# Optimization experiments

Hardware: AMD Instinct MI355X
Metric: run time of the kernel (lower is better)

The kernel has to match this reference:

```python
import math
import jax, jax.numpy as jnp
import numpy as np

SEQ, BATCH, HID, N_HEAD = 1024, 8, 1024, 16


def setup_inputs() -> dict:
    key0 = jax.random.key(0)
    ks = jax.random.split(key0, 7)
    shp = (SEQ, BATCH, HID)
    w = lambda k: jax.random.normal(k, (HID, HID), dtype=jnp.float32) * 0.02
    return {
        "value": jax.random.normal(ks[0], shp, dtype=jnp.float32),
        "key": jax.random.normal(ks[1], shp, dtype=jnp.float32),
        "query": jax.random.normal(ks[2], shp, dtype=jnp.float32),
        "Wq": w(ks[3]), "Wk": w(ks[4]), "Wv": w(ks[5]), "Wo": w(ks[6]),
    }


def _proj_split(x, W, n_head, d_k):
    # x: (S,B,H) -> linear -> split heads -> stack heads along batch dim: (S, n_head*B, d_k)
    S, B, H = x.shape
    p = x @ W.T                                   # (S,B,H)
    p = p.reshape(S, B, n_head, d_k)
    p = p.transpose(0, 2, 1, 3).reshape(S, n_head * B, d_k)
    return p


def reference(value, key, query, Wq, Wk, Wv, Wo):
    S, B, H = value.shape
    n_head = N_HEAD
    d_k = H // n_head
    Q = _proj_split(query, Wq, n_head, d_k)       # (S, n_head*B, d_k)
    K = _proj_split(key, Wk, n_head, d_k)
    V = _proj_split(value, Wv, n_head, d_k)
    # scores[b,i,j] = K_i . Q_j / sqrt(d_k)  (note: rows = key index, cols = query index)
    scores = jnp.einsum('ibd,jbd->bij', K, Q) / math.sqrt(d_k)  # (n_head*B, S, S)
    future_mask = jnp.triu(jnp.ones((S, S), dtype=bool), 1)      # True where j > i
    scores = jnp.where(future_mask[None, :, :], -jnp.inf, scores)
    # faithful to original: softmax over dim=2 (the QUERY axis)
    dist = jax.nn.softmax(scores, axis=2)                         # (n_head*B, S, S)
    # att[j,b,d] = sum_i dist[b,i,j] * V[i,b,d]
    att = jnp.einsum('bij,ibd->jbd', dist, V)                     # (S, n_head*B, d_k)
    # un-stack heads: (S, n_head, B, d_k) -> (B, S, n_head*d_k)
    att = att.reshape(S, n_head, B, d_k).transpose(2, 0, 1, 3).reshape(B, S, H)
    out = (att @ Wo.T).transpose(1, 0, 2)                         # (S, B, H)
    return out, dist
```

## Files before the change

### kernel.cpp

```cpp
#include <hip/hip_runtime.h>
#include <hip/hip_bf16.h>
#include <stdint.h>

#define SQ   1024
#define NB   8
#define HD   1024
#define NHD  16
#define DKK  64

typedef __bf16 bf16x8_t __attribute__((ext_vector_type(8)));
typedef float  f32x4_t  __attribute__((ext_vector_type(4)));
typedef __hip_bfloat16 bf16;

__device__ __forceinline__ void gld_lds16(const void* g, void* l) {
    __builtin_amdgcn_global_load_lds(
        (__attribute__((address_space(1))) void*)const_cast<void*>(g),
        (__attribute__((address_space(3))) void*)l,
        16, 0, 0);
}

__device__ __forceinline__ bf16x8_t cvt8(float4 a, float4 b) {
    bf16x8_t r;
    r[0] = (__bf16)a.x; r[1] = (__bf16)a.y; r[2] = (__bf16)a.z; r[3] = (__bf16)a.w;
    r[4] = (__bf16)b.x; r[5] = (__bf16)b.y; r[6] = (__bf16)b.z; r[7] = (__bf16)b.w;
    return r;
}

__global__ __launch_bounds__(256, 2)
void gemm_kernel(const void* __restrict__ A0, const void* __restrict__ A1,
                 const void* __restrict__ A2,
                 const float* __restrict__ W0, const float* __restrict__ W1,
                 const float* __restrict__ W2,
                 void* __restrict__ O0, void* __restrict__ O1,
                 void* __restrict__ O2, int mode)
{
    const int z = blockIdx.z;
    const void*  A  = (z == 0) ? A0 : (z == 1) ? A1 : A2;
    const float* Wf = (z == 0) ? W0 : (z == 1) ? W1 : W2;
    void*        Ov = (z == 0) ? O0 : (z == 1) ? O1 : O2;

    __shared__ alignas(16) bf16 lA[128 * 32];
    __shared__ alignas(16) bf16 lB[128 * 32];

    const int tid  = threadIdx.x;
    const int lane = tid & 63;
    const int w    = tid >> 6;
    const int wr   = w >> 1;
    const int wc   = w & 1;
    const int g    = lane >> 4;
    const int ln   = lane & 15;
    const int bm   = blockIdx.y;
    const int bn   = blockIdx.x;

    f32x4_t acc[4][4];
#pragma unroll
    for (int i = 0; i < 4; ++i)
#pragma unroll
        for (int j = 0; j < 4; ++j)
            acc[i][j] = (f32x4_t){0.f, 0.f, 0.f, 0.f};

    const size_t arow0 = (size_t)bm * 128;
    const size_t brow0 = (size_t)bn * 128;
    const float* Af  = (const float*)A;
    const bf16*  Ab  = (const bf16*)A;

    for (int k0 = 0; k0 < HD; k0 += 32) {
#pragma unroll
        for (int q = 0; q < 2; ++q) {
            const int cid = (q * 4 + w) * 64 + lane;
            const int r   = cid >> 2;
            const int gch = (cid & 3) ^ ((r ^ (r >> 2)) & 3);
            if (mode == 0) {
                const float4* src = (const float4*)(Af + (arow0 + r) * HD + k0 + gch * 8);
                *(bf16x8_t*)&lA[cid * 8] = cvt8(src[0], src[1]);
            } else {
                gld_lds16((const char*)Ab + ((arow0 + r) * HD + k0) * 2 + gch * 16,
                          (char*)lA + cid * 16);
            }
            const float4* wsrc = (const float4*)(Wf + (brow0 + r) * HD + k0 + gch * 8);
            *(bf16x8_t*)&lB[cid * 8] = cvt8(wsrc[0], wsrc[1]);
        }
        __syncthreads();
        bf16x8_t av[4], bv[4];
#pragma unroll
        for (int mi = 0; mi < 4; ++mi) {
            const int row = wr * 64 + mi * 16 + ln;
            av[mi] = *(const bf16x8_t*)&lA[row * 32 + ((g ^ ((row ^ (row >> 2)) & 3)) << 3)];
        }
#pragma unroll
        for (int ni = 0; ni < 4; ++ni) {
            const int row = wc * 64 + ni * 16 + ln;
            bv[ni] = *(const bf16x8_t*)&lB[row * 32 + ((g ^ ((row ^ (row >> 2)) & 3)) << 3)];
        }
#pragma unroll
        for (int mi = 0; mi < 4; ++mi)
#pragma unroll
            for (int ni = 0; ni < 4; ++ni)
                acc[mi][ni] = __builtin_amdgcn_mfma_f32_16x16x32_bf16(
                    av[mi], bv[ni], acc[mi][ni], 0, 0, 0);
        __syncthreads();
    }

    bf16*  Ob = (bf16*)Ov;
    float* Of = (float*)Ov;
#pragma unroll
    for (int mi = 0; mi < 4; ++mi) {
#pragma unroll
        for (int ni = 0; ni < 4; ++ni) {
            const int o = bn * 128 + wc * 64 + ni * 16 + ln;
#pragma unroll
            for (int r = 0; r < 4; ++r) {
                const int m = bm * 128 + wr * 64 + mi * 16 + g * 4 + r;
                const float v = acc[mi][ni][r];
                if (mode == 0) {
                    const int h = o >> 6, d = o & 63;
                    const int s = m >> 3, b = m & 7;
                    Ob[(((size_t)(h * 8 + b) * SQ + s) << 6) + d] = __float2bfloat16(v);
                } else {
                    Of[(size_t)m * HD + o] = v;
                }
            }
        }
    }
}

__global__ __launch_bounds__(256, 2)
void scores_softmax_kernel(const bf16* __restrict__ Kh, const bf16* __restrict__ Qh,
                           float* __restrict__ Dist)
{
    __shared__ alignas(16) bf16 Kl[64 * 64];
    __shared__ alignas(16) bf16 Ql[64 * 64];
    const int tid = threadIdx.x, lane = tid & 63, w = tid >> 6;
    const int g = lane >> 4, ln = lane & 15;
    const int ib = blockIdx.x, bh = blockIdx.y;
    const char* Kp = (const char*)(Kh + ((size_t)bh * SQ + ib * 64) * DKK);
    const char* Qp = (const char*)(Qh + (size_t)bh * SQ * DKK);
    float* Dp = Dist + (size_t)bh * SQ * SQ;

#pragma unroll
    for (int q = 0; q < 2; ++q) {
        const int cid = (q * 4 + w) * 64 + lane;
        const int r   = cid >> 3;
        const int cc  = (cid & 7) ^ ((r ^ (r >> 3)) & 7);
        gld_lds16(Kp + r * 128 + cc * 16, (char*)Kl + cid * 16);
    }
    __syncthreads();
    const int arow = w * 16 + ln;
    const int asw  = (arow ^ (arow >> 3)) & 7;
    const bf16x8_t ak0 = *(const bf16x8_t*)&Kl[arow * 64 + ((g ^ asw) << 3)];
    const bf16x8_t ak1 = *(const bf16x8_t*)&Kl[arow * 64 + (((4 + g) ^ asw) << 3)];

    const int irow = ib * 64 + w * 16 + g * 4;

    auto stage_q = [&](int jt) {
#pragma unroll
        for (int q = 0; q < 2; ++q) {
            const int cid = (q * 4 + w) * 64 + lane;
            const int r   = cid >> 3;
            const int cc  = (cid & 7) ^ ((r ^ (r >> 3)) & 7);
            gld_lds16(Qp + (size_t)jt * 8192 + r * 128 + cc * 16, (char*)Ql + cid * 16);
        }
    };
    auto compute_tile = [&](f32x4_t* accp) {
#pragma unroll
        for (int nf = 0; nf < 4; ++nf) {
            const int brow = nf * 16 + ln;
            const int bsw  = (brow ^ (brow >> 3)) & 7;
            bf16x8_t b0 = *(const bf16x8_t*)&Ql[brow * 64 + ((g ^ bsw) << 3)];
            bf16x8_t b1 = *(const bf16x8_t*)&Ql[brow * 64 + (((4 + g) ^ bsw) << 3)];
            f32x4_t a = (f32x4_t){0.f, 0.f, 0.f, 0.f};
            a = __builtin_amdgcn_mfma_f32_16x16x32_bf16(ak0, b0, a, 0, 0, 0);
            a = __builtin_amdgcn_mfma_f32_16x16x32_bf16(ak1, b1, a, 0, 0, 0);
            accp[nf] = a;
        }
    };

    float lsum[4] = {0.f, 0.f, 0.f, 0.f};
    for (int jt = 0; jt <= ib; ++jt) {
        __syncthreads();
        stage_q(jt);
        __syncthreads();
        f32x4_t acc[4];
        compute_tile(acc);
        float part[4] = {0.f, 0.f, 0.f, 0.f};
#pragma unroll
        for (int nf = 0; nf < 4; ++nf) {
            const int j = jt * 64 + nf * 16 + ln;
#pragma unroll
            for (int r = 0; r < 4; ++r) {
                const float s = acc[nf][r] * 0.125f;
                part[r] += (j <= irow + r) ? __expf(s) : 0.f;
            }
        }
#pragma unroll
        for (int r = 0; r < 4; ++r) {
            float p = part[r];
            p += __shfl_xor(p, 1);
            p += __shfl_xor(p, 2);
            p += __shfl_xor(p, 4);
            p += __shfl_xor(p, 8);
            lsum[r] += p;
        }
    }
    float inv[4];
#pragma unroll
    for (int r = 0; r < 4; ++r) inv[r] = 1.f / lsum[r];

    for (int jt = 0; jt < 16; ++jt) {
        if (jt <= ib) {
            __syncthreads();
            stage_q(jt);
            __syncthreads();
            f32x4_t acc[4];
            compute_tile(acc);
#pragma unroll
            for (int nf = 0; nf < 4; ++nf) {
                const int j = jt * 64 + nf * 16 + ln;
#pragma unroll
                for (int r = 0; r < 4; ++r) {
                    const float e = (j <= irow + r)
                        ? __expf(acc[nf][r] * 0.125f) * inv[r] : 0.f;
                    Dp[(size_t)(irow + r) * SQ + j] = e;
                }
            }
        } else {
            const uint4 zz = make_uint4(0u, 0u, 0u, 0u);
#pragma unroll
            for (int q = 0; q < 4; ++q) {
                const int cid = q * 256 + tid;
                const int row = cid >> 4;
                float* p = Dp + (size_t)(ib * 64 + row) * SQ + jt * 64 + (cid & 15) * 4;
                *(uint4*)p = zz;
            }
        }
    }
}

__global__ __launch_bounds__(256, 2)
void att_v_kernel(const float* __restrict__ Dist, const bf16* __restrict__ Vh,
                  bf16* __restrict__ att4)
{
    __shared__ alignas(16) bf16 dT[64 * 72];
    __shared__ alignas(16) bf16 vT[64 * 72];
    const int tid = threadIdx.x, lane = tid & 63, w = tid >> 6;
    const int g = lane >> 4, ln = lane & 15;
    const int jb = blockIdx.x, bh = blockIdx.y;
    const float* Dp = Dist + (size_t)bh * SQ * SQ;
    const bf16*  Vp = Vh + (size_t)bh * SQ * DKK;

    f32x4_t acc[4];
#pragma unroll
    for (int nf = 0; nf < 4; ++nf) acc[nf] = (f32x4_t){0.f, 0.f, 0.f, 0.f};

    unsigned short* dTs = (unsigned short*)dT;
    unsigned short* vTs = (unsigned short*)vT;

    for (int it = jb; it < 16; ++it) {
        __syncthreads();
#pragma unroll
        for (int q = 0; q < 4; ++q) {
            const int cid = q * 256 + tid;
            const int i   = cid >> 4;
            const int jc  = (cid & 15) * 4;
            float4 dv = *(const float4*)(Dp + ((size_t)(it * 64 + i) * SQ + jb * 64 + jc));
            const float de[4] = {dv.x, dv.y, dv.z, dv.w};
#pragma unroll
            for (int e = 0; e < 4; ++e) {
                const int j   = jc + e;
                const int isw = i ^ (((j >> 3) & 7) << 3);
                bf16 bv = __float2bfloat16(de[e]);
                dTs[j * 72 + isw] = *(unsigned short*)&bv;
            }
        }
#pragma unroll
        for (int q = 0; q < 2; ++q) {
            const int cid = q * 256 + tid;
            const int i   = cid >> 3;
            const int dc  = (cid & 7) * 8;
            uint4 vvec = *(const uint4*)(Vp + ((size_t)(it * 64 + i) * DKK + dc));
            const unsigned short* vs = (const unsigned short*)&vvec;
#pragma unroll
            for (int e = 0; e < 8; ++e) {
                const int d   = dc + e;
                const int isw = i ^ (((d >> 3) & 7) << 3);
                vTs[d * 72 + isw] = vs[e];
            }
        }
        __syncthreads();
#pragma unroll
        for (int kk = 0; kk < 2; ++kk) {
            const int arow  = w * 16 + ln;
            const int abase = (kk * 32 + g * 8) ^ (((arow >> 3) & 7) << 3);
            bf16x8_t a = *(const bf16x8_t*)&dT[arow * 72 + abase];
#pragma unroll
            for (int nf = 0; nf < 4; ++nf) {
                const int brow  = nf * 16 + ln;
                const int bbase = (kk * 32 + g * 8) ^ (((brow >> 3) & 7) << 3);
                bf16x8_t b = *(const bf16x8_t*)&vT[brow * 72 + bbase];
                acc[nf] = __builtin_amdgcn_mfma_f32_16x16x32_bf16(a, b, acc[nf], 0, 0, 0);
            }
        }
    }
    const int h = bh >> 3, b = bh & 7;
#pragma unroll
    for (int nf = 0; nf < 4; ++nf) {
#pragma unroll
        for (int r = 0; r < 4; ++r) {
            const int j = jb * 64 + w * 16 + g * 4 + r;
            att4[(size_t)(j * 8 + b) * HD + h * 64 + nf * 16 + ln] =
                __float2bfloat16(acc[nf][r]);
        }
    }
}

extern "C" void kernel_launch(void* const* d_in, const int* in_sizes, int n_in,
                              void* d_out, int out_size, void* d_ws, size_t ws_size,
                              hipStream_t stream)
{
    const float* value = (const float*)d_in[0];
    const float* key_  = (const float*)d_in[1];
    const float* query = (const float*)d_in[2];
    const float* Wq    = (const float*)d_in[3];
    const float* Wk    = (const float*)d_in[4];
    const float* Wv    = (const float*)d_in[5];
    const float* Wo    = (const float*)d_in[6];

    float* out  = (float*)d_out;
    float* dist = out + (size_t)SQ * NB * HD;

    char* ws   = (char*)d_ws;
    bf16* Qh   = (bf16*)(ws);
    bf16* Kh   = (bf16*)(ws + (size_t)16 * 1024 * 1024);
    bf16* Vh   = (bf16*)(ws + (size_t)32 * 1024 * 1024);
    bf16* att4 = (bf16*)(ws + (size_t)48 * 1024 * 1024);

    dim3 blk(256);
    gemm_kernel<<<dim3(8, 64, 3), blk, 0, stream>>>(
        query, key_, value, Wq, Wk, Wv, Qh, Kh, Vh, 0);
    scores_softmax_kernel<<<dim3(16, 128), blk, 0, stream>>>(Kh, Qh, dist);
    att_v_kernel<<<dim3(16, 128), blk, 0, stream>>>(dist, Vh, att4);
    gemm_kernel<<<dim3(8, 64, 1), blk, 0, stream>>>(
        att4, att4, att4, Wo, Wo, Wo, out, out, out, 1);
}
```

Measured before the change: 1.007 ms.

## Fuse dist computation with PV, double-buffer GEMM and attention staging

The separate scores+softmax write and att_v read of the fp32 dist matrix are replaced by a rowsum kernel that computes only inverse row sums, plus a fused kernel that recomputes scores per column block, writes dist, and immediately multiplies by V through LDS. V is stored transposed by the projection GEMM, so the PV kernel can stage it without a per-element transpose. The GEMM gains register-prefetched double buffering, and the attention kernels double-buffer Q/K/V tiles. The cost is recomputing the QK scores and more LDS per block. The inverse row sums are parked in the output buffer, which the final GEMM later overwrites.

```diff
diff --git a/kernel.cpp b/kernel.cpp
--- a/kernel.cpp
+++ b/kernel.cpp
@@ -9,6 +9,7 @@
 #define DKK  64
 
 typedef __bf16 bf16x8_t __attribute__((ext_vector_type(8)));
+typedef __bf16 bf16x4_t __attribute__((ext_vector_type(4)));
 typedef float  f32x4_t  __attribute__((ext_vector_type(4)));
 typedef __hip_bfloat16 bf16;
 
@@ -24,6 +25,17 @@
     r[0] = (__bf16)a.x; r[1] = (__bf16)a.y; r[2] = (__bf16)a.z; r[3] = (__bf16)a.w;
     r[4] = (__bf16)b.x; r[5] = (__bf16)b.y; r[6] = (__bf16)b.z; r[7] = (__bf16)b.w;
     return r;
+}
+
+__device__ __forceinline__ void stage64(const char* gbase, int rowstride,
+                                        char* lbase, int w, int lane) {
+#pragma unroll
+    for (int q = 0; q < 2; ++q) {
+        const int cid = (q * 4 + w) * 64 + lane;
+        const int r   = cid >> 3;
+        const int cc  = (cid & 7) ^ ((r ^ (r >> 3)) & 7);
+        gld_lds16(gbase + r * rowstride + cc * 16, lbase + cid * 16);
+    }
 }
 
 __global__ __launch_bounds__(256, 2)
@@ -39,8 +51,8 @@
     const float* Wf = (z == 0) ? W0 : (z == 1) ? W1 : W2;
     void*        Ov = (z == 0) ? O0 : (z == 1) ? O1 : O2;
 
-    __shared__ alignas(16) bf16 lA[128 * 32];
-    __shared__ alignas(16) bf16 lB[128 * 32];
+    __shared__ alignas(16) bf16 lA[2][128 * 32];
+    __shared__ alignas(16) bf16 lB[2][128 * 32];
 
     const int tid  = threadIdx.x;
     const int lane = tid & 63;
@@ -61,36 +73,69 @@
 
     const size_t arow0 = (size_t)bm * 128;
     const size_t brow0 = (size_t)bn * 128;
-    const float* Af  = (const float*)A;
-    const bf16*  Ab  = (const bf16*)A;
-
-    for (int k0 = 0; k0 < HD; k0 += 32) {
+    const float* Af = (const float*)A;
+    const bf16*  Ab = (const bf16*)A;
+
+    int scid[2], srow[2], sch[2];
+#pragma unroll
+    for (int q = 0; q < 2; ++q) {
+        const int cid = (q * 4 + w) * 64 + lane;
+        scid[q] = cid;
+        srow[q] = cid >> 2;
+        sch[q]  = (cid & 3) ^ ((srow[q] ^ (srow[q] >> 2)) & 3);
+    }
+
+    float4 pa[4], pw[4];
+
+    auto issue_loads = [&](int k0, int buf) {
 #pragma unroll
         for (int q = 0; q < 2; ++q) {
-            const int cid = (q * 4 + w) * 64 + lane;
-            const int r   = cid >> 2;
-            const int gch = (cid & 3) ^ ((r ^ (r >> 2)) & 3);
-            if (mode == 0) {
-                const float4* src = (const float4*)(Af + (arow0 + r) * HD + k0 + gch * 8);
-                *(bf16x8_t*)&lA[cid * 8] = cvt8(src[0], src[1]);
-            } else {
-                gld_lds16((const char*)Ab + ((arow0 + r) * HD + k0) * 2 + gch * 16,
-                          (char*)lA + cid * 16);
+            const float4* wsrc = (const float4*)(Wf + (brow0 + srow[q]) * HD + k0 + sch[q] * 8);
+            pw[q * 2]     = wsrc[0];
+            pw[q * 2 + 1] = wsrc[1];
+        }
+        if (mode == 0) {
+#pragma unroll
+            for (int q = 0; q < 2; ++q) {
+                const float4* asrc = (const float4*)(Af + (arow0 + srow[q]) * HD + k0 + sch[q] * 8);
+                pa[q * 2]     = asrc[0];
+                pa[q * 2 + 1] = asrc[1];
             }
-            const float4* wsrc = (const float4*)(Wf + (brow0 + r) * HD + k0 + gch * 8);
-            *(bf16x8_t*)&lB[cid * 8] = cvt8(wsrc[0], wsrc[1]);
-        }
-        __syncthreads();
+        } else {
+#pragma unroll
+            for (int q = 0; q < 2; ++q)
+                gld_lds16((const char*)Ab + ((arow0 + srow[q]) * HD + k0) * 2 + sch[q] * 16,
+                          (char*)&lA[buf][0] + scid[q] * 16);
+        }
+    };
+    auto commit_writes = [&](int buf) {
+#pragma unroll
+        for (int q = 0; q < 2; ++q)
+            *(bf16x8_t*)&lB[buf][scid[q] * 8] = cvt8(pw[q * 2], pw[q * 2 + 1]);
+        if (mode == 0) {
+#pragma unroll
+            for (int q = 0; q < 2; ++q)
+                *(bf16x8_t*)&lA[buf][scid[q] * 8] = cvt8(pa[q * 2], pa[q * 2 + 1]);
+        }
+    };
+
+    issue_loads(0, 0);
+    commit_writes(0);
+    __syncthreads();
+
+    int cur = 0;
+    for (int ks = 0; ks < 32; ++ks) {
+        if (ks < 31) issue_loads((ks + 1) * 32, cur ^ 1);
         bf16x8_t av[4], bv[4];
 #pragma unroll
         for (int mi = 0; mi < 4; ++mi) {
             const int row = wr * 64 + mi * 16 + ln;
-            av[mi] = *(const bf16x8_t*)&lA[row * 32 + ((g ^ ((row ^ (row >> 2)) & 3)) << 3)];
+            av[mi] = *(const bf16x8_t*)&lA[cur][row * 32 + ((g ^ ((row ^ (row >> 2)) & 3)) << 3)];
         }
 #pragma unroll
         for (int ni = 0; ni < 4; ++ni) {
             const int row = wc * 64 + ni * 16 + ln;
-            bv[ni] = *(const bf16x8_t*)&lB[row * 32 + ((g ^ ((row ^ (row >> 2)) & 3)) << 3)];
+            bv[ni] = *(const bf16x8_t*)&lB[cur][row * 32 + ((g ^ ((row ^ (row >> 2)) & 3)) << 3)];
         }
 #pragma unroll
         for (int mi = 0; mi < 4; ++mi)
@@ -98,7 +143,9 @@
             for (int ni = 0; ni < 4; ++ni)
                 acc[mi][ni] = __builtin_amdgcn_mfma_f32_16x16x32_bf16(
                     av[mi], bv[ni], acc[mi][ni], 0, 0, 0);
+        if (ks < 31) commit_writes(cur ^ 1);
         __syncthreads();
+        cur ^= 1;
     }
 
     bf16*  Ob = (bf16*)Ov;
@@ -115,7 +162,10 @@
                 if (mode == 0) {
                     const int h = o >> 6, d = o & 63;
                     const int s = m >> 3, b = m & 7;
-                    Ob[(((size_t)(h * 8 + b) * SQ + s) << 6) + d] = __float2bfloat16(v);
+                    if (z == 2)
+                        Ob[((size_t)((h * 8 + b) * DKK + d)) * SQ + s] = __float2bfloat16(v);
+                    else
+                        Ob[(((size_t)(h * 8 + b) * SQ + s) << 6) + d] = __float2bfloat16(v);
                 } else {
                     Of[(size_t)m * HD + o] = v;
                 }
@@ -125,72 +175,46 @@
 }
 
 __global__ __launch_bounds__(256, 2)
-void scores_softmax_kernel(const bf16* __restrict__ Kh, const bf16* __restrict__ Qh,
-                           float* __restrict__ Dist)
+void rowsum_kernel(const bf16* __restrict__ Kh, const bf16* __restrict__ Qh,
+                   float* __restrict__ invS)
 {
     __shared__ alignas(16) bf16 Kl[64 * 64];
-    __shared__ alignas(16) bf16 Ql[64 * 64];
+    __shared__ alignas(16) bf16 Ql[2][64 * 64];
     const int tid = threadIdx.x, lane = tid & 63, w = tid >> 6;
     const int g = lane >> 4, ln = lane & 15;
-    const int ib = blockIdx.x, bh = blockIdx.y;
+    const int ib = 15 - (int)blockIdx.x, bh = blockIdx.y;
     const char* Kp = (const char*)(Kh + ((size_t)bh * SQ + ib * 64) * DKK);
     const char* Qp = (const char*)(Qh + (size_t)bh * SQ * DKK);
-    float* Dp = Dist + (size_t)bh * SQ * SQ;
-
-#pragma unroll
-    for (int q = 0; q < 2; ++q) {
-        const int cid = (q * 4 + w) * 64 + lane;
-        const int r   = cid >> 3;
-        const int cc  = (cid & 7) ^ ((r ^ (r >> 3)) & 7);
-        gld_lds16(Kp + r * 128 + cc * 16, (char*)Kl + cid * 16);
-    }
+
+    stage64(Kp, 128, (char*)Kl, w, lane);
+    stage64(Qp, 128, (char*)Ql[0], w, lane);
     __syncthreads();
+
     const int arow = w * 16 + ln;
     const int asw  = (arow ^ (arow >> 3)) & 7;
     const bf16x8_t ak0 = *(const bf16x8_t*)&Kl[arow * 64 + ((g ^ asw) << 3)];
     const bf16x8_t ak1 = *(const bf16x8_t*)&Kl[arow * 64 + (((4 + g) ^ asw) << 3)];
-
     const int irow = ib * 64 + w * 16 + g * 4;
 
-    auto stage_q = [&](int jt) {
-#pragma unroll
-        for (int q = 0; q < 2; ++q) {
-            const int cid = (q * 4 + w) * 64 + lane;
-            const int r   = cid >> 3;
-            const int cc  = (cid & 7) ^ ((r ^ (r >> 3)) & 7);
-            gld_lds16(Qp + (size_t)jt * 8192 + r * 128 + cc * 16, (char*)Ql + cid * 16);
-        }
-    };
-    auto compute_tile = [&](f32x4_t* accp) {
+    float lsum[4] = {0.f, 0.f, 0.f, 0.f};
+    int cur = 0;
+    for (int jt = 0; jt <= ib; ++jt) {
+        if (jt < ib)
+            stage64(Qp + (size_t)(jt + 1) * 8192, 128, (char*)Ql[cur ^ 1], w, lane);
+        float part[4] = {0.f, 0.f, 0.f, 0.f};
 #pragma unroll
         for (int nf = 0; nf < 4; ++nf) {
             const int brow = nf * 16 + ln;
             const int bsw  = (brow ^ (brow >> 3)) & 7;
-            bf16x8_t b0 = *(const bf16x8_t*)&Ql[brow * 64 + ((g ^ bsw) << 3)];
-            bf16x8_t b1 = *(const bf16x8_t*)&Ql[brow * 64 + (((4 + g) ^ bsw) << 3)];
+            bf16x8_t b0 = *(const bf16x8_t*)&Ql[cur][brow * 64 + ((g ^ bsw) << 3)];
+            bf16x8_t b1 = *(const bf16x8_t*)&Ql[cur][brow * 64 + (((4 + g) ^ bsw) << 3)];
             f32x4_t a = (f32x4_t){0.f, 0.f, 0.f, 0.f};
             a = __builtin_amdgcn_mfma_f32_16x16x32_bf16(ak0, b0, a, 0, 0, 0);
             a = __builtin_amdgcn_mfma_f32_16x16x32_bf16(ak1, b1, a, 0, 0, 0);
-            accp[nf] = a;
-        }
-    };
-
-    float lsum[4] = {0.f, 0.f, 0.f, 0.f};
-    for (int jt = 0; jt <= ib; ++jt) {
-        __syncthreads();
-        stage_q(jt);
-        __syncthreads();
-        f32x4_t acc[4];
-        compute_tile(acc);
-        float part[4] = {0.f, 0.f, 0.f, 0.f};
-#pragma unroll
-        for (int nf = 0; nf < 4; ++nf) {
             const int j = jt * 64 + nf * 16 + ln;
 #pragma unroll
-            for (int r = 0; r < 4; ++r) {
-                const float s = acc[nf][r] * 0.125f;
-                part[r] += (j <= irow + r) ? __expf(s) : 0.f;
-            }
+            for (int r = 0; r < 4; ++r)
+                part[r] += (j <= irow + r) ? __expf(a[r] * 0.125f) : 0.f;
         }
 #pragma unroll
         for (int r = 0; r < 4; ++r) {
@@ -201,106 +225,112 @@
             p += __shfl_xor(p, 8);
             lsum[r] += p;
         }
-    }
-    float inv[4];
-#pragma unroll
-    for (int r = 0; r < 4; ++r) inv[r] = 1.f / lsum[r];
-
-    for (int jt = 0; jt < 16; ++jt) {
-        if (jt <= ib) {
-            __syncthreads();
-            stage_q(jt);
-            __syncthreads();
-            f32x4_t acc[4];
-            compute_tile(acc);
-#pragma unroll
-            for (int nf = 0; nf < 4; ++nf) {
-                const int j = jt * 64 + nf * 16 + ln;
-#pragma unroll
-                for (int r = 0; r < 4; ++r) {
-                    const float e = (j <= irow + r)
-                        ? __expf(acc[nf][r] * 0.125f) * inv[r] : 0.f;
-                    Dp[(size_t)(irow + r) * SQ + j] = e;
-                }
-            }
-        } else {
-            const uint4 zz = make_uint4(0u, 0u, 0u, 0u);
-#pragma unroll
-            for (int q = 0; q < 4; ++q) {
-                const int cid = q * 256 + tid;
-                const int row = cid >> 4;
-                float* p = Dp + (size_t)(ib * 64 + row) * SQ + jt * 64 + (cid & 15) * 4;
-                *(uint4*)p = zz;
-            }
-        }
+        __syncthreads();
+        cur ^= 1;
+    }
+    if (ln == 0) {
+#pragma unroll
+        for (int r = 0; r < 4; ++r)
+            invS[(size_t)bh * SQ + irow + r] = 1.f / lsum[r];
     }
 }
 
 __global__ __launch_bounds__(256, 2)
-void att_v_kernel(const float* __restrict__ Dist, const bf16* __restrict__ Vh,
-                  bf16* __restrict__ att4)
+void dist_pv_kernel(const bf16* __restrict__ Kh, const bf16* __restrict__ Qh,
+                    const bf16* __restrict__ Vt, const float* __restrict__ invS,
+                    float* __restrict__ Dist, bf16* __restrict__ att4)
 {
+    __shared__ alignas(16) bf16 Kl[2][64 * 64];
+    __shared__ alignas(16) bf16 Vl[2][64 * 64];
+    __shared__ alignas(16) bf16 Ql[64 * 64];
     __shared__ alignas(16) bf16 dT[64 * 72];
-    __shared__ alignas(16) bf16 vT[64 * 72];
     const int tid = threadIdx.x, lane = tid & 63, w = tid >> 6;
     const int g = lane >> 4, ln = lane & 15;
     const int jb = blockIdx.x, bh = blockIdx.y;
-    const float* Dp = Dist + (size_t)bh * SQ * SQ;
-    const bf16*  Vp = Vh + (size_t)bh * SQ * DKK;
-
-    f32x4_t acc[4];
-#pragma unroll
-    for (int nf = 0; nf < 4; ++nf) acc[nf] = (f32x4_t){0.f, 0.f, 0.f, 0.f};
-
-    unsigned short* dTs = (unsigned short*)dT;
-    unsigned short* vTs = (unsigned short*)vT;
-
-    for (int it = jb; it < 16; ++it) {
-        __syncthreads();
+    const char* Kp = (const char*)(Kh + (size_t)bh * SQ * DKK);
+    const char* Qp = (const char*)(Qh + (size_t)bh * SQ * DKK);
+    const char* Vp = (const char*)(Vt + (size_t)bh * DKK * SQ);
+    float* Dp = Dist + (size_t)bh * SQ * SQ;
+    const float* ivp = invS + (size_t)bh * SQ;
+
+    stage64(Qp + (size_t)jb * 8192, 128, (char*)Ql, w, lane);
+    __syncthreads();
+    bf16x8_t bq[4][2];
+#pragma unroll
+    for (int nf = 0; nf < 4; ++nf) {
+        const int brow = nf * 16 + ln;
+        const int bsw  = (brow ^ (brow >> 3)) & 7;
+        bq[nf][0] = *(const bf16x8_t*)&Ql[brow * 64 + ((g ^ bsw) << 3)];
+        bq[nf][1] = *(const bf16x8_t*)&Ql[brow * 64 + (((4 + g) ^ bsw) << 3)];
+    }
+
+    stage64(Kp + (size_t)jb * 8192, 128, (char*)Kl[0], w, lane);
+    stage64(Vp + (size_t)jb * 128, 2048, (char*)Vl[0], w, lane);
+
+    const f32x4_t zero4 = (f32x4_t){0.f, 0.f, 0.f, 0.f};
+    for (int it0 = 0; it0 < jb; ++it0) {
 #pragma unroll
         for (int q = 0; q < 4; ++q) {
             const int cid = q * 256 + tid;
-            const int i   = cid >> 4;
-            const int jc  = (cid & 15) * 4;
-            float4 dv = *(const float4*)(Dp + ((size_t)(it * 64 + i) * SQ + jb * 64 + jc));
-            const float de[4] = {dv.x, dv.y, dv.z, dv.w};
-#pragma unroll
-            for (int e = 0; e < 4; ++e) {
-                const int j   = jc + e;
-                const int isw = i ^ (((j >> 3) & 7) << 3);
-                bf16 bv = __float2bfloat16(de[e]);
-                dTs[j * 72 + isw] = *(unsigned short*)&bv;
+            const int row = cid >> 4, ch = cid & 15;
+            *(f32x4_t*)(Dp + (size_t)(it0 * 64 + row) * SQ + jb * 64 + ch * 4) = zero4;
+        }
+    }
+    __syncthreads();
+
+    const int arow = w * 16 + ln;
+    const int asw  = (arow ^ (arow >> 3)) & 7;
+    f32x4_t accPV[4];
+#pragma unroll
+    for (int nf = 0; nf < 4; ++nf) accPV[nf] = zero4;
+
+    int cur = 0;
+    for (int it = jb; it < 16; ++it) {
+        if (it < 15) {
+            stage64(Kp + (size_t)(it + 1) * 8192, 128, (char*)Kl[cur ^ 1], w, lane);
+            stage64(Vp + (size_t)(it + 1) * 128, 2048, (char*)Vl[cur ^ 1], w, lane);
+        }
+        const int i0 = it * 64 + w * 16 + g * 4;
+        float iv[4];
+#pragma unroll
+        for (int r = 0; r < 4; ++r) iv[r] = ivp[i0 + r];
+
+        const bf16x8_t ak0 = *(const bf16x8_t*)&Kl[cur][arow * 64 + ((g ^ asw) << 3)];
+        const bf16x8_t ak1 = *(const bf16x8_t*)&Kl[cur][arow * 64 + (((4 + g) ^ asw) << 3)];
+#pragma unroll
+        for (int nf = 0; nf < 4; ++nf) {
+            f32x4_t a = zero4;
+            a = __builtin_amdgcn_mfma_f32_16x16x32_bf16(ak0, bq[nf][0], a, 0, 0, 0);
+            a = __builtin_amdgcn_mfma_f32_16x16x32_bf16(ak1, bq[nf][1], a, 0, 0, 0);
+            const int jl = nf * 16 + ln;
+            const int j  = jb * 64 + jl;
+            bf16x4_t pk;
+#pragma unroll
+            for (int r = 0; r < 4; ++r) {
+                const float e = (j <= i0 + r) ? __expf(a[r] * 0.125f) * iv[r] : 0.f;
+                Dp[(size_t)(i0 + r) * SQ + j] = e;
+                pk[r] = (__bf16)e;
             }
-        }
-#pragma unroll
-        for (int q = 0; q < 2; ++q) {
-            const int cid = q * 256 + tid;
-            const int i   = cid >> 3;
-            const int dc  = (cid & 7) * 8;
-            uint4 vvec = *(const uint4*)(Vp + ((size_t)(it * 64 + i) * DKK + dc));
-            const unsigned short* vs = (const unsigned short*)&vvec;
-#pragma unroll
-            for (int e = 0; e < 8; ++e) {
-                const int d   = dc + e;
-                const int isw = i ^ (((d >> 3) & 7) << 3);
-                vTs[d * 72 + isw] = vs[e];
+            *(bf16x4_t*)&dT[jl * 72 + ((w * 16 + g * 4) ^ (((jl >> 3) & 7) << 3))] = pk;
+        }
+        __syncthreads();
+#pragma unroll
+        for (int kk = 0; kk < 2; ++kk) {
+            const int abase = (kk * 32 + g * 8) ^ (((arow >> 3) & 7) << 3);
+            const bf16x8_t a = *(const bf16x8_t*)&dT[arow * 72 + abase];
+#pragma unroll
+            for (int nf = 0; nf < 4; ++nf) {
+                const int brow = nf * 16 + ln;
+                const int bsw  = (brow ^ (brow >> 3)) & 7;
+                const bf16x8_t b =
+                    *(const bf16x8_t*)&Vl[cur][brow * 64 + (((kk * 4 + g) ^ bsw) << 3)];
+                accPV[nf] = __builtin_amdgcn_mfma_f32_16x16x32_bf16(a, b, accPV[nf], 0, 0, 0);
             }
         }
         __syncthreads();
-#pragma unroll
-        for (int kk = 0; kk < 2; ++kk) {
-            const int arow  = w * 16 + ln;
-            const int abase = (kk * 32 + g * 8) ^ (((arow >> 3) & 7) << 3);
-            bf16x8_t a = *(const bf16x8_t*)&dT[arow * 72 + abase];
-#pragma unroll
-            for (int nf = 0; nf < 4; ++nf) {
-                const int brow  = nf * 16 + ln;
-                const int bbase = (kk * 32 + g * 8) ^ (((brow >> 3) & 7) << 3);
-                bf16x8_t b = *(const bf16x8_t*)&vT[brow * 72 + bbase];
-                acc[nf] = __builtin_amdgcn_mfma_f32_16x16x32_bf16(a, b, acc[nf], 0, 0, 0);
-            }
-        }
-    }
+        cur ^= 1;
+    }
+
     const int h = bh >> 3, b = bh & 7;
 #pragma unroll
     for (int nf = 0; nf < 4; ++nf) {
@@ -308,7 +338,7 @@
         for (int r = 0; r < 4; ++r) {
             const int j = jb * 64 + w * 16 + g * 4 + r;
             att4[(size_t)(j * 8 + b) * HD + h * 64 + nf * 16 + ln] =
-                __float2bfloat16(acc[nf][r]);
+                __float2bfloat16(accPV[nf][r]);
         }
     }
 }
@@ -327,18 +357,19 @@
 
     float* out  = (float*)d_out;
     float* dist = out + (size_t)SQ * NB * HD;
+    float* invS = out;
 
     char* ws   = (char*)d_ws;
     bf16* Qh   = (bf16*)(ws);
     bf16* Kh   = (bf16*)(ws + (size_t)16 * 1024 * 1024);
-    bf16* Vh   = (bf16*)(ws + (size_t)32 * 1024 * 1024);
+    bf16* Vt   = (bf16*)(ws + (size_t)32 * 1024 * 1024);
     bf16* att4 = (bf16*)(ws + (size_t)48 * 1024 * 1024);
 
     dim3 blk(256);
     gemm_kernel<<<dim3(8, 64, 3), blk, 0, stream>>>(
-        query, key_, value, Wq, Wk, Wv, Qh, Kh, Vh, 0);
-    scores_softmax_kernel<<<dim3(16, 128), blk, 0, stream>>>(Kh, Qh, dist);
-    att_v_kernel<<<dim3(16, 128), blk, 0, stream>>>(dist, Vh, att4);
+        query, key_, value, Wq, Wk, Wv, Qh, Kh, Vt, 0);
+    rowsum_kernel<<<dim3(16, 128), blk, 0, stream>>>(Kh, Qh, invS);
+    dist_pv_kernel<<<dim3(16, 128), blk, 0, stream>>>(Kh, Qh, Vt, invS, dist, att4);
     gemm_kernel<<<dim3(8, 64, 1), blk, 0, stream>>>(
         att4, att4, att4, Wo, Wo, Wo, out, out, out, 1);
 }
```

After: 952.8 us. 5.4% less time.
